# Performance work log

Hardware: AMD Instinct MI355X
Metric: run time of the kernel (lower is better)

The kernel has to match this reference:

```python
import jax, jax.numpy as jnp
import numpy as np

OUT, IN = 5632, 2048
GROUP_SIZE = 128
N_GROUPS = (OUT * IN) // GROUP_SIZE
LORA_SCALE = 32.0 / 16.0  # lora_alpha / lora_r


def dequantize_int4(packed, scales, zeros):
    # packed: [numel//2], each byte holds two 4-bit codes (low nibble first)
    low = packed & 0xF
    high = (packed >> 4) & 0xF
    q = jnp.stack([low, high], axis=-1).reshape(-1).astype(jnp.float32)  # [numel]
    q = q.reshape(N_GROUPS, GROUP_SIZE)
    w = (q - zeros[:, None]) * scales[:, None]
    return w.reshape(OUT, IN)


def setup_inputs() -> dict:
    key = jax.random.key(0)
    k1, k2, k3, k4, k5, k6 = jax.random.split(key, 6)
    x = jax.random.normal(k1, (4, 2048, IN), dtype=jnp.float32)
    packed = jax.random.randint(k2, ((OUT * IN) // 2,), 0, 256, dtype=jnp.int32)
    scales = jax.random.uniform(k3, (N_GROUPS,), dtype=jnp.float32) * 0.02 + 1e-3
    zeros = jax.random.uniform(k4, (N_GROUPS,), dtype=jnp.float32) * 15.0
    lora_A = jax.random.normal(k5, (IN, 16), dtype=jnp.float32) * (1.0 / np.sqrt(IN))
    lora_B = jax.random.normal(k6, (16, OUT), dtype=jnp.float32) * 0.02
    return {"x": x, "packed": packed, "scales": scales, "zeros": zeros,
            "lora_A": lora_A, "lora_B": lora_B}


def reference(x, packed, scales, zeros, lora_A, lora_B):
    W = dequantize_int4(packed, scales, zeros)            # [OUT, IN]
    base = jnp.einsum('bsi,oi->bso', x, W)                # F.linear(x, W)
    lora = ((x @ lora_A) @ lora_B) * LORA_SCALE           # low-rank path
    return base + lora
```

## Files before the change

### kernel.cpp

```cpp
#include <hip/hip_runtime.h>

#define M_DIM 8192
#define K_DIM 2048
#define N_DIM 5632

typedef __attribute__((ext_vector_type(8))) short short8;
typedef __attribute__((ext_vector_type(4))) float f32x4;

__device__ __forceinline__ short f2b(float f) {
  union { float f; unsigned u; } v; v.f = f;
  unsigned r = v.u + 0x7FFFu + ((v.u >> 16) & 1u);
  return (short)(r >> 16);
}

__device__ __forceinline__ void async16(void* lds, const void* g) {
  __builtin_amdgcn_global_load_lds(
      (const __attribute__((address_space(1))) unsigned*)g,
      (__attribute__((address_space(3))) unsigned*)lds,
      16, 0, 0);
}

__global__ __launch_bounds__(256) void cvt_x_kernel(const float* __restrict__ x,
                                                    short* __restrict__ xb) {
  long t = (long)blockIdx.x * 256 + threadIdx.x;
  const float4* xv = (const float4*)x;
  float4 f0 = xv[2 * t];
  float4 f1 = xv[2 * t + 1];
  short8 o;
  o[0] = f2b(f0.x); o[1] = f2b(f0.y); o[2] = f2b(f0.z); o[3] = f2b(f0.w);
  o[4] = f2b(f1.x); o[5] = f2b(f1.y); o[6] = f2b(f1.z); o[7] = f2b(f1.w);
  *(short8*)(xb + 8 * t) = o;
}

__global__ __launch_bounds__(256) void dequant_lora_kernel(
    const int* __restrict__ packed, const float* __restrict__ scales,
    const float* __restrict__ zeros, const float* __restrict__ lA,
    const float* __restrict__ lB, short* __restrict__ wb) {
  int o = blockIdx.x;
  int i0 = threadIdx.x * 8;
  long e0 = (long)o * K_DIM + i0;
  int4 p = ((const int4*)packed)[e0 >> 3];
  int g = (int)(e0 >> 7);
  float s = scales[g], z = zeros[g];

  float bcol[16];
#pragma unroll
  for (int r = 0; r < 16; ++r) bcol[r] = lB[r * N_DIM + o] * 2.0f;

  short8 out8;
#pragma unroll
  for (int d = 0; d < 4; ++d) {
    int pv = (&p.x)[d];
    float w0 = ((float)(pv & 0xF) - z) * s;
    float w1 = ((float)((pv >> 4) & 0xF) - z) * s;
    const float4* a0 = (const float4*)&lA[(i0 + 2 * d) * 16];
    const float4* a1 = (const float4*)&lA[(i0 + 2 * d + 1) * 16];
    float acc0 = 0.f, acc1 = 0.f;
#pragma unroll
    for (int r4 = 0; r4 < 4; ++r4) {
      float4 av0 = a0[r4], av1 = a1[r4];
      acc0 += av0.x * bcol[4 * r4] + av0.y * bcol[4 * r4 + 1] +
              av0.z * bcol[4 * r4 + 2] + av0.w * bcol[4 * r4 + 3];
      acc1 += av1.x * bcol[4 * r4] + av1.y * bcol[4 * r4 + 1] +
              av1.z * bcol[4 * r4 + 2] + av1.w * bcol[4 * r4 + 3];
    }
    out8[2 * d] = f2b(w0 + acc0);
    out8[2 * d + 1] = f2b(w1 + acc1);
  }
  *(short8*)(wb + e0) = out8;
}

__global__ __launch_bounds__(256) void gemm_kernel(const short* __restrict__ xb,
                                                   const short* __restrict__ wb,
                                                   float* __restrict__ out) {
  __shared__ __align__(16) short As[128 * 64];
  __shared__ __align__(16) short Bs[128 * 64];

  const int tid = threadIdx.x;
  const int wave = tid >> 6, lane = tid & 63;
  const int wm = wave >> 1, wn = wave & 1;
  const int l15 = lane & 15, quad = lane >> 4;
  const int m0 = blockIdx.y * 128, n0 = blockIdx.x * 128;
  const short* a_base = xb + (size_t)m0 * K_DIM;
  const short* b_base = wb + (size_t)n0 * K_DIM;

  f32x4 acc[4][4] = {};

  int a_off[2][4], b_off[2][4];
#pragma unroll
  for (int ks = 0; ks < 2; ++ks) {
    int c = ks * 4 + quad;
#pragma unroll
    for (int i = 0; i < 4; ++i) {
      int ra = wm * 64 + i * 16 + l15;
      int rb = wn * 64 + i * 16 + l15;
      a_off[ks][i] = (ra * 8 + (c ^ (ra & 7))) * 8;
      b_off[ks][i] = (rb * 8 + (c ^ (rb & 7))) * 8;
    }
  }

  for (int k0 = 0; k0 < K_DIM; k0 += 64) {
    __syncthreads();
#pragma unroll
    for (int it = 0; it < 4; ++it) {
      int gi = it * 256 + tid;
      int row = gi >> 3;
      int c = (gi & 7) ^ (row & 7);
      async16(&As[gi * 8], a_base + (size_t)row * K_DIM + k0 + c * 8);
      async16(&Bs[gi * 8], b_base + (size_t)row * K_DIM + k0 + c * 8);
    }
    __syncthreads();

#pragma unroll
    for (int ks = 0; ks < 2; ++ks) {
      short8 af[4], bf[4];
#pragma unroll
      for (int mi = 0; mi < 4; ++mi) af[mi] = *(const short8*)&As[a_off[ks][mi]];
#pragma unroll
      for (int ni = 0; ni < 4; ++ni) bf[ni] = *(const short8*)&Bs[b_off[ks][ni]];
#pragma unroll
      for (int mi = 0; mi < 4; ++mi)
#pragma unroll
        for (int ni = 0; ni < 4; ++ni)
          acc[mi][ni] = __builtin_amdgcn_mfma_f32_16x16x32_bf16(
              af[mi], bf[ni], acc[mi][ni], 0, 0, 0);
    }
  }

  float* op = out + (size_t)(m0 + wm * 64 + quad * 4) * N_DIM + n0 + wn * 64 + l15;
#pragma unroll
  for (int mi = 0; mi < 4; ++mi)
#pragma unroll
    for (int r = 0; r < 4; ++r)
#pragma unroll
      for (int ni = 0; ni < 4; ++ni)
        op[(size_t)(mi * 16 + r) * N_DIM + ni * 16] = acc[mi][ni][r];
}

extern "C" void kernel_launch(void* const* d_in, const int* in_sizes, int n_in,
                              void* d_out, int out_size, void* d_ws, size_t ws_size,
                              hipStream_t stream) {
  const float* x      = (const float*)d_in[0];
  const int*   packed = (const int*)d_in[1];
  const float* scales = (const float*)d_in[2];
  const float* zeros  = (const float*)d_in[3];
  const float* lA     = (const float*)d_in[4];
  const float* lB     = (const float*)d_in[5];
  float* out = (float*)d_out;

  short* xb = (short*)d_ws;
  short* wb = xb + (size_t)M_DIM * K_DIM;

  cvt_x_kernel<<<(M_DIM * K_DIM) / (256 * 8), 256, 0, stream>>>(x, xb);
  dequant_lora_kernel<<<N_DIM, 256, 0, stream>>>(packed, scales, zeros, lA, lB, wb);
  gemm_kernel<<<dim3(N_DIM / 128, M_DIM / 128), 256, 0, stream>>>(xb, wb, out);
}
```

Measured before the change: 561.6 us.

## Merge prep kernels and remap GEMM tiles for better L2 locality

Fuses the x-to-bf16 conversion and the dequant+LoRA weight kernel into one launch, using block index ranges to select the role. The GEMM moves to a 1D grid with a custom mapping that groups tiles by N-strip and M-half, likely to improve L2/XCD reuse of the A and B tiles. Address computation for the async LDS loads is also hoisted into a precomputed per-thread offset. The tile remap changes the schedule order and may help or hurt cache behaviour depending on how the hardware distributes blocks across XCDs.

```diff
diff --git a/kernel.cpp b/kernel.cpp
--- a/kernel.cpp
+++ b/kernel.cpp
@@ -20,23 +20,24 @@
       16, 0, 0);
 }
 
-__global__ __launch_bounds__(256) void cvt_x_kernel(const float* __restrict__ x,
-                                                    short* __restrict__ xb) {
-  long t = (long)blockIdx.x * 256 + threadIdx.x;
-  const float4* xv = (const float4*)x;
-  float4 f0 = xv[2 * t];
-  float4 f1 = xv[2 * t + 1];
-  short8 o;
-  o[0] = f2b(f0.x); o[1] = f2b(f0.y); o[2] = f2b(f0.z); o[3] = f2b(f0.w);
-  o[4] = f2b(f1.x); o[5] = f2b(f1.y); o[6] = f2b(f1.z); o[7] = f2b(f1.w);
-  *(short8*)(xb + 8 * t) = o;
-}
-
-__global__ __launch_bounds__(256) void dequant_lora_kernel(
-    const int* __restrict__ packed, const float* __restrict__ scales,
-    const float* __restrict__ zeros, const float* __restrict__ lA,
-    const float* __restrict__ lB, short* __restrict__ wb) {
-  int o = blockIdx.x;
+#define CVT_BLOCKS 8192
+__global__ __launch_bounds__(256) void prep_kernel(
+    const float* __restrict__ x, const int* __restrict__ packed,
+    const float* __restrict__ scales, const float* __restrict__ zeros,
+    const float* __restrict__ lA, const float* __restrict__ lB,
+    short* __restrict__ xb, short* __restrict__ wb) {
+  if (blockIdx.x < CVT_BLOCKS) {
+    long t = (long)blockIdx.x * 256 + threadIdx.x;
+    const float4* xv = (const float4*)x;
+    float4 f0 = xv[2 * t];
+    float4 f1 = xv[2 * t + 1];
+    short8 o;
+    o[0] = f2b(f0.x); o[1] = f2b(f0.y); o[2] = f2b(f0.z); o[3] = f2b(f0.w);
+    o[4] = f2b(f1.x); o[5] = f2b(f1.y); o[6] = f2b(f1.z); o[7] = f2b(f1.w);
+    *(short8*)(xb + 8 * t) = o;
+    return;
+  }
+  int o = blockIdx.x - CVT_BLOCKS;
   int i0 = threadIdx.x * 8;
   long e0 = (long)o * K_DIM + i0;
   int4 p = ((const int4*)packed)[e0 >> 3];
@@ -80,9 +81,20 @@
   const int wave = tid >> 6, lane = tid & 63;
   const int wm = wave >> 1, wn = wave & 1;
   const int l15 = lane & 15, quad = lane >> 4;
-  const int m0 = blockIdx.y * 128, n0 = blockIdx.x * 128;
+
+  int bid = blockIdx.x;
+  int t = bid >> 3;
+  int strip = bid & 3, half = (bid >> 2) & 1;
+  int xt = strip * 11 + (t >> 5);
+  int yt = half * 32 + (t & 31);
+  const int m0 = yt * 128, n0 = xt * 128;
+
   const short* a_base = xb + (size_t)m0 * K_DIM;
   const short* b_base = wb + (size_t)n0 * K_DIM;
+
+  const unsigned r0 = tid >> 3;
+  const unsigned cc = ((tid & 7) ^ (r0 & 7)) * 8;
+  const unsigned vOff = r0 * K_DIM + cc;
 
   f32x4 acc[4][4] = {};
 
@@ -103,11 +115,10 @@
     __syncthreads();
 #pragma unroll
     for (int it = 0; it < 4; ++it) {
-      int gi = it * 256 + tid;
-      int row = gi >> 3;
-      int c = (gi & 7) ^ (row & 7);
-      async16(&As[gi * 8], a_base + (size_t)row * K_DIM + k0 + c * 8);
-      async16(&Bs[gi * 8], b_base + (size_t)row * K_DIM + k0 + c * 8);
+      async16(&As[it * 2048 + tid * 8],
+              a_base + (size_t)(it * 32 * K_DIM + k0) + vOff);
+      async16(&Bs[it * 2048 + tid * 8],
+              b_base + (size_t)(it * 32 * K_DIM + k0) + vOff);
     }
     __syncthreads();
 
@@ -151,7 +162,7 @@
   short* xb = (short*)d_ws;
   short* wb = xb + (size_t)M_DIM * K_DIM;
 
-  cvt_x_kernel<<<(M_DIM * K_DIM) / (256 * 8), 256, 0, stream>>>(x, xb);
-  dequant_lora_kernel<<<N_DIM, 256, 0, stream>>>(packed, scales, zeros, lA, lB, wb);
-  gemm_kernel<<<dim3(N_DIM / 128, M_DIM / 128), 256, 0, stream>>>(xb, wb, out);
+  prep_kernel<<<CVT_BLOCKS + N_DIM, 256, 0, stream>>>(x, packed, scales, zeros,
+                                                      lA, lB, xb, wb);
+  gemm_kernel<<<(N_DIM / 128) * (M_DIM / 128), 256, 0, stream>>>(xb, wb, out);
 }
```

Measured after the change: 577.4 us. 2.8% more time.
